# Kernel optimization log

Measured on AMD Instinct MI355X. Metric: run time of the kernel, lower is better.

The kernel has to match this reference:

```python
import jax, jax.numpy as jnp
import numpy as np


def gconv(feat, src, dst, w, n):
    # sparse weighted aggregation: out[i] = sum_{(j->i) in E} w_e * feat[j]
    return jax.ops.segment_sum(feat[src] * w[:, None], dst, num_segments=n)


def tgcn_cell(x, h, src, dst, w, Wg, bg, Wc, bc):
    n = x.shape[0]
    # gates: r, z = sigmoid(GC([x, h]) @ Wg + bg)
    a = gconv(jnp.concatenate([x, h], axis=-1), src, dst, w, n)
    rz = jax.nn.sigmoid(a @ Wg + bg)
    r, z = jnp.split(rz, 2, axis=-1)
    # candidate: c = tanh(GC([x, r*h]) @ Wc + bc)
    b = gconv(jnp.concatenate([x, r * h], axis=-1), src, dst, w, n)
    c = jnp.tanh(b @ Wc + bc)
    return z * h + (1.0 - z) * c


def setup_inputs() -> dict:
    key = jax.random.key(0)
    ks = jax.random.split(key, 8)
    N, F, T, H, E, OUT = 50000, 8, 12, 64, 800000, 1
    x = jax.random.normal(ks[0], (N, F, T), dtype=jnp.float32)
    edge_index = jax.random.randint(ks[1], (2, E), 0, N, dtype=jnp.int32)
    edge_weight = jax.random.uniform(ks[2], (E,), dtype=jnp.float32)
    init = lambda k, shp, fan: (jax.random.normal(k, shp, jnp.float32) / np.sqrt(fan)).astype(jnp.float32)
    Wg0 = init(ks[3], (F + H, 2 * H), F + H); bg0 = jnp.zeros((2 * H,), jnp.float32)
    Wc0 = init(ks[4], (F + H, H), F + H);     bc0 = jnp.zeros((H,), jnp.float32)
    Wg1 = init(ks[5], (2 * H, 2 * H), 2 * H); bg1 = jnp.zeros((2 * H,), jnp.float32)
    Wc1 = init(ks[6], (2 * H, H), 2 * H);     bc1 = jnp.zeros((H,), jnp.float32)
    Wout = init(ks[7], (H, OUT), H);          bout = jnp.zeros((OUT,), jnp.float32)
    return dict(x=x, edge_index=edge_index, edge_weight=edge_weight,
                Wg0=Wg0, bg0=bg0, Wc0=Wc0, bc0=bc0,
                Wg1=Wg1, bg1=bg1, Wc1=Wc1, bc1=bc1,
                Wout=Wout, bout=bout)


def reference(x, edge_index, edge_weight, Wg0, bg0, Wc0, bc0,
              Wg1, bg1, Wc1, bc1, Wout, bout):
    src, dst = edge_index[0], edge_index[1]
    n = x.shape[0]
    H = Wc0.shape[1]
    xt = jnp.transpose(x, (2, 0, 1))  # (T, N, F)
    h_init = (jnp.zeros((n, H), x.dtype), jnp.zeros((n, H), x.dtype))

    def step(carry, x_t):
        h0, h1 = carry
        h0 = tgcn_cell(x_t, h0, src, dst, edge_weight, Wg0, bg0, Wc0, bc0)
        h1 = tgcn_cell(h0, h1, src, dst, edge_weight, Wg1, bg1, Wc1, bc1)
        return (h0, h1), None

    (_, h1_final), _ = jax.lax.scan(step, h_init, xt)
    return h1_final @ Wout + bout  # (N, OUT); Identity output activation
```

## Files before the change

kernel.cpp:

```cpp
#include <hip/hip_runtime.h>
#include <hip/hip_fp16.h>


#define FT 96
#define TSTEPS 12

typedef _Float16 f16x8 __attribute__((ext_vector_type(8)));
typedef float f32x4 __attribute__((ext_vector_type(4)));

static __device__ __forceinline__ float lo2f(unsigned v) {
    __half2 h2 = *reinterpret_cast<const __half2*>(&v);
    return __low2float(h2);
}
static __device__ __forceinline__ float hi2f(unsigned v) {
    __half2 h2 = *reinterpret_cast<const __half2*>(&v);
    return __high2float(h2);
}
static __device__ __forceinline__ float wof(unsigned p) {
    return __half2float(__ushort_as_half((unsigned short)(p >> 16)));
}

__global__ void hist_k(const int* __restrict__ dst, int* __restrict__ deg, int E) {
    int e = blockIdx.x * blockDim.x + threadIdx.x;
    if (e < E) atomicAdd(&deg[dst[e]], 1);
}

__global__ __launch_bounds__(256) void partial_k(const int* __restrict__ deg,
                                                 int* __restrict__ part, int N) {
    __shared__ int sm[256];
    int i = blockIdx.x * 256 + threadIdx.x;
    sm[threadIdx.x] = (i < N) ? deg[i] : 0;
    __syncthreads();
    for (int off = 128; off > 0; off >>= 1) {
        if (threadIdx.x < off) sm[threadIdx.x] += sm[threadIdx.x + off];
        __syncthreads();
    }
    if (threadIdx.x == 0) part[blockIdx.x] = sm[0];
}

__global__ __launch_bounds__(256) void scanpart_k(int* __restrict__ part,
                                                  int* __restrict__ rowptr,
                                                  int G, int N) {
    __shared__ int sm[256];
    int v = (threadIdx.x < G) ? part[threadIdx.x] : 0;
    sm[threadIdx.x] = v;
    __syncthreads();
    for (int off = 1; off < 256; off <<= 1) {
        int t = (threadIdx.x >= (unsigned)off) ? sm[threadIdx.x - off] : 0;
        __syncthreads();
        sm[threadIdx.x] += t;
        __syncthreads();
    }
    if (threadIdx.x < G) part[threadIdx.x] = sm[threadIdx.x] - v;
    if (threadIdx.x == 255) rowptr[N] = sm[255];
}

__global__ __launch_bounds__(256) void scanchunk_k(const int* __restrict__ deg,
                                                   const int* __restrict__ part,
                                                   int* __restrict__ rowptr,
                                                   int* __restrict__ cursor, int N) {
    __shared__ int sm[256];
    int i = blockIdx.x * 256 + threadIdx.x;
    int v = (i < N) ? deg[i] : 0;
    sm[threadIdx.x] = v;
    __syncthreads();
    for (int off = 1; off < 256; off <<= 1) {
        int t = (threadIdx.x >= (unsigned)off) ? sm[threadIdx.x - off] : 0;
        __syncthreads();
        sm[threadIdx.x] += t;
        __syncthreads();
    }
    int excl = sm[threadIdx.x] - v + part[blockIdx.x];
    if (i < N) { rowptr[i] = excl; cursor[i] = excl; }
}

__global__ void fill_k(const int* __restrict__ src, const int* __restrict__ dst,
                       const float* __restrict__ ew, int* __restrict__ cursor,
                       unsigned* __restrict__ csr_ew, int E) {
    int e = blockIdx.x * blockDim.x + threadIdx.x;
    if (e >= E) return;
    int pos = atomicAdd(&cursor[dst[e]], 1);
    unsigned hw = (unsigned)__half_as_ushort(__float2half(ew[e]));
    csr_ew[pos] = (unsigned)src[e] | (hw << 16);
}

__global__ void x2h_k(const float* __restrict__ x, _Float16* __restrict__ xh, int M) {
    int i = blockIdx.x * blockDim.x + threadIdx.x;
    if (i < M) xh[i] = (_Float16)x[i];
}

__global__ void wprep_k(const float* __restrict__ Wg0, const float* __restrict__ Wc0,
                        const float* __restrict__ Wg1, const float* __restrict__ Wc1,
                        _Float16* __restrict__ Wg1t, _Float16* __restrict__ Wc1t,
                        _Float16* __restrict__ Wc0t, _Float16* __restrict__ Wg0t_h,
                        _Float16* __restrict__ Wg0t_x) {
    int i = blockIdx.x * 256 + threadIdx.x;
    if (i < 128 * 128) { int c = i >> 7, k = i & 127; Wg1t[i] = (_Float16)Wg1[k * 128 + c]; }
    if (i < 64 * 128)  { int c = i >> 7, k = i & 127; Wc1t[i] = (_Float16)Wc1[k * 64 + c]; }
    if (i < 64 * 96)   { int c = i / 96, k = i - c * 96;
                         Wc0t[i] = (k < 72) ? (_Float16)Wc0[k * 64 + c] : (_Float16)0.f; }
    if (i < 128 * 64)  { int c = i >> 6, k = i & 63; Wg0t_h[i] = (_Float16)Wg0[(8 + k) * 128 + c]; }
    if (i < 128 * 32)  { int c = i >> 5, k = i & 31;
                         Wg0t_x[i] = (k < 8) ? (_Float16)Wg0[k * 128 + c] : (_Float16)0.f; }
}

__global__ __launch_bounds__(256) void gather96_k(
    const _Float16* __restrict__ xh, const int* __restrict__ rowptr,
    const unsigned* __restrict__ csr_ew, float* __restrict__ aggXt, int N) {
    int n = blockIdx.x * 4 + (threadIdx.x >> 6);
    if (n >= N) return;
    int c = threadIdx.x & 63;
    int beg = rowptr[n], end = rowptr[n + 1];
    int deg = end - beg;
    float a0 = 0.f, a1 = 0.f;
    unsigned ev = 0;
    if (c < deg) ev = csr_ew[beg + c];
    int m = deg < 64 ? deg : 64;
    int m8 = (m + 7) & ~7;
#pragma unroll 8
    for (int j = 0; j < m8; ++j) {
        unsigned p = __shfl(ev, j);
        int s = p & 0xffff;
        float w = wof(p);
        const _Float16* row = xh + (size_t)s * FT;
        a0 = fmaf(w, (float)row[c], a0);
        if (c < 32) a1 = fmaf(w, (float)row[64 + c], a1);
    }
    for (int e = beg + 64; e < end; ++e) {
        unsigned p = csr_ew[e];
        int s = p & 0xffff;
        float w = wof(p);
        const _Float16* row = xh + (size_t)s * FT;
        a0 = fmaf(w, (float)row[c], a0);
        if (c < 32) a1 = fmaf(w, (float)row[64 + c], a1);
    }
    { int f = c / 12, tt = c - f * 12;
      aggXt[((size_t)tt * N + n) * 8 + f] = a0; }
    if (c < 32) { int cc = 64 + c; int f = cc / 12, tt = cc - f * 12;
      aggXt[((size_t)tt * N + n) * 8 + f] = a1; }
}

__global__ void g0z_k(const float* __restrict__ aggXt, const float* __restrict__ Wg0,
                      const float* __restrict__ bg0, _Float16* __restrict__ Zh, int N) {
    int i = blockIdx.x * blockDim.x + threadIdx.x;
    int n = i >> 6;
    if (n >= N) return;
    int c = i & 63;
    float acc = bg0[64 + c];
#pragma unroll
    for (int f = 0; f < 8; ++f) acc += aggXt[(size_t)n * 8 + f] * Wg0[f * 128 + 64 + c];
    Zh[(size_t)n * 64 + c] = (_Float16)(1.f / (1.f + __expf(-acc)));
}

__device__ __forceinline__ void gpair16(const unsigned* __restrict__ feat32,
    const unsigned* __restrict__ csr_ew,
    int begA, int degA, int begB, int degB, int lane,
    float& o0, float& o1) {
    const int half = lane >> 5, c2 = lane & 31;
    const int beg = half ? begB : begA;
    const int deg = half ? degB : degA;
    const int m = deg < 32 ? deg : 32;
    unsigned ev = 0;
    if (c2 < m) ev = csr_ew[beg + c2];
    int dmax = degA > degB ? degA : degB;
    int jm = dmax < 32 ? dmax : 32;
    jm = (jm + 15) & ~15;
    float a0 = 0.f, a1 = 0.f;
    const int base = half << 5;
    for (int j = 0; j < jm; j += 16) {
        unsigned vv[16]; float ww[16];
#pragma unroll
        for (int k = 0; k < 16; ++k) {
            unsigned p = __shfl(ev, base + j + k);
            ww[k] = wof(p);
            vv[k] = feat32[(size_t)(p & 0xffff) * 32 + c2];
        }
#pragma unroll
        for (int k = 0; k < 16; ++k) {
            a0 = fmaf(ww[k], lo2f(vv[k]), a0);
            a1 = fmaf(ww[k], hi2f(vv[k]), a1);
        }
    }
    int end = beg + deg;
    for (int e = beg + 32; e < end; ++e) {
        unsigned p = csr_ew[e];
        float w = wof(p);
        unsigned v = feat32[(size_t)(p & 0xffff) * 32 + c2];
        a0 = fmaf(w, lo2f(v), a0);
        a1 = fmaf(w, hi2f(v), a1);
    }
    o0 = a0; o1 = a1;
}

__global__ __launch_bounds__(512) void l0_cand(
    const _Float16* __restrict__ RH0h, const float* __restrict__ aggXt, int t,
    const int* __restrict__ rowptr, const unsigned* __restrict__ csr_ew,
    const _Float16* __restrict__ Wc0t, const float* __restrict__ bc,
    const _Float16* __restrict__ Zh, float* __restrict__ h0f,
    unsigned* __restrict__ h01, int N) {
    __shared__ _Float16 sA[64 * 104];
    const int tid = threadIdx.x;
    const int lane = tid & 63;
    const int wid = __builtin_amdgcn_readfirstlane(tid >> 6);
    const int nb = blockIdx.x * 64;
    { int nl = tid >> 3, k0 = 72 + ((tid & 7) << 2);
#pragma unroll
      for (int q = 0; q < 4; ++q) sA[nl * 104 + k0 + q] = (_Float16)0.f; }
    { int nl = tid >> 3, f = tid & 7, n = nb + nl;
      sA[nl * 104 + f] = (n < N) ? (_Float16)aggXt[((size_t)t * N + n) * 8 + f] : (_Float16)0.f; }
    for (int i = 0; i < 4; ++i) {
        int pr = wid * 4 + i;
        int nlA = pr * 2, nlB = nlA + 1;
        int nA = nb + nlA, nB = nb + nlB;
        int begA = 0, degA = 0, begB = 0, degB = 0;
        if (nA < N) { begA = rowptr[nA]; degA = rowptr[nA + 1] - begA; }
        if (nB < N) { begB = rowptr[nB]; degB = rowptr[nB + 1] - begB; }
        float o0, o1;
        gpair16((const unsigned*)RH0h, csr_ew, begA, degA, begB, degB, lane, o0, o1);
        int nl = (lane < 32) ? nlA : nlB;
        int c2 = lane & 31;
        sA[nl * 104 + 8 + 2 * c2] = (_Float16)o0;
        sA[nl * 104 + 8 + 2 * c2 + 1] = (_Float16)o1;
    }
    __syncthreads();
    const int ln15 = lane & 15, quad = lane >> 4;
    const int mt = wid & 3, ng = wid >> 2;
    const int mrow = mt * 16 + ln15;
    f16x8 afr[3];
#pragma unroll
    for (int kc = 0; kc < 3; ++kc)
        afr[kc] = *(const f16x8*)&sA[mrow * 104 + kc * 32 + quad * 8];
    f32x4 acc[2];
    int cols[2];
#pragma unroll
    for (int nt = 0; nt < 2; ++nt) {
        int col = (ng * 2 + nt) * 16 + ln15;
        cols[nt] = col;
        float b = bc[col];
        f32x4 a = {b, b, b, b};
#pragma unroll
        for (int kc = 0; kc < 3; ++kc) {
            f16x8 bfr = *(const f16x8*)&Wc0t[(size_t)col * 96 + kc * 32 + quad * 8];
            a = __builtin_amdgcn_mfma_f32_16x16x32_f16(afr[kc], bfr, a, 0, 0, 0);
        }
        acc[nt] = a;
    }
    __syncthreads();
#pragma unroll
    for (int nt = 0; nt < 2; ++nt) {
#pragma unroll
        for (int r = 0; r < 4; ++r) {
            float e = __expf(2.f * acc[nt][r]);
            float c = 1.f - 2.f / (e + 1.f);
            int row = mt * 16 + quad * 4 + r;
            sA[row * 104 + cols[nt]] = (_Float16)c;
        }
    }
    __syncthreads();
    for (int i = tid; i < 4096; i += 512) {
        int nl = i >> 6, cc = i & 63, n = nb + nl;
        if (n < N) {
            size_t idx = (size_t)n * 64 + cc;
            float z = (float)Zh[idx];
            float hv = h0f[idx];
            float nh = z * hv + (1.f - z) * (float)sA[nl * 104 + cc];
            h0f[idx] = nh;
            reinterpret_cast<__half*>(h01)[idx * 2] = __float2half(nh);
        }
    }
}

__global__ __launch_bounds__(512) void l1_gate(
    const unsigned* __restrict__ h01, const float* __restrict__ h1f,
    const int* __restrict__ rowptr, const unsigned* __restrict__ csr_ew,
    const _Float16* __restrict__ Wg1t, const float* __restrict__ bg,
    unsigned* __restrict__ Aglobh32, _Float16* __restrict__ Zh,
    _Float16* __restrict__ RH1h, int N) {
    __shared__ _Float16 sA[64 * 136];
    const int tid = threadIdx.x;
    const int lane = tid & 63;
    const int wid = __builtin_amdgcn_readfirstlane(tid >> 6);
    const int nb = blockIdx.x * 64;
    const uint2* __restrict__ f2 = (const uint2*)h01;
    for (int i = 0; i < 4; ++i) {
        int pr = wid * 4 + i;
        int nlA = pr * 2, nlB = nlA + 1;
        int nA = nb + nlA, nB = nb + nlB;
        int begA = 0, degA = 0, begB = 0, degB = 0;
        if (nA < N) { begA = rowptr[nA]; degA = rowptr[nA + 1] - begA; }
        if (nB < N) { begB = rowptr[nB]; degB = rowptr[nB + 1] - begB; }
        const int half = lane >> 5, c2 = lane & 31;
        const int beg = half ? begB : begA;
        const int deg = half ? degB : degA;
        const int m = deg < 32 ? deg : 32;
        unsigned ev = 0;
        if (c2 < m) ev = csr_ew[beg + c2];
        int dmax = degA > degB ? degA : degB;
        int jm = dmax < 32 ? dmax : 32;
        jm = (jm + 7) & ~7;
        float p00 = 0.f, p01 = 0.f, p10 = 0.f, p11 = 0.f;
        const int base = half << 5;
        for (int j = 0; j < jm; j += 8) {
            uint2 vv[8]; float ww[8];
#pragma unroll
            for (int k = 0; k < 8; ++k) {
                unsigned p = __shfl(ev, base + j + k);
                ww[k] = wof(p);
                vv[k] = f2[(size_t)(p & 0xffff) * 32 + c2];
            }
#pragma unroll
            for (int k = 0; k < 8; ++k) {
                p00 = fmaf(ww[k], lo2f(vv[k].x), p00);
                p10 = fmaf(ww[k], hi2f(vv[k].x), p10);
                p01 = fmaf(ww[k], lo2f(vv[k].y), p01);
                p11 = fmaf(ww[k], hi2f(vv[k].y), p11);
            }
        }
        int end = beg + deg;
        for (int e = beg + 32; e < end; ++e) {
            unsigned p = csr_ew[e];
            float w = wof(p);
            uint2 v = f2[(size_t)(p & 0xffff) * 32 + c2];
            p00 = fmaf(w, lo2f(v.x), p00);
            p10 = fmaf(w, hi2f(v.x), p10);
            p01 = fmaf(w, lo2f(v.y), p01);
            p11 = fmaf(w, hi2f(v.y), p11);
        }
        int nl = (lane < 32) ? nlA : nlB;
        int c2w = lane & 31;
        sA[nl * 136 + 2 * c2w] = (_Float16)p00;
        sA[nl * 136 + 2 * c2w + 1] = (_Float16)p01;
        sA[nl * 136 + 64 + 2 * c2w] = (_Float16)p10;
        sA[nl * 136 + 64 + 2 * c2w + 1] = (_Float16)p11;
    }
    __syncthreads();
    for (int i = tid; i < 2048; i += 512) {
        int nl = i >> 5, c2 = i & 31, n = nb + nl;
        if (n < N) Aglobh32[(size_t)n * 32 + c2] = ((const unsigned*)sA)[nl * 68 + c2];
    }
    const int ln15 = lane & 15, quad = lane >> 4;
    const int mt = wid & 3, ng = wid >> 2;
    const int mrow = mt * 16 + ln15;
    f16x8 afr[4];
#pragma unroll
    for (int kc = 0; kc < 4; ++kc)
        afr[kc] = *(const f16x8*)&sA[mrow * 136 + kc * 32 + quad * 8];
    f32x4 acc[4];
    int cols[4];
#pragma unroll
    for (int nt = 0; nt < 4; ++nt) {
        int col = (ng * 4 + nt) * 16 + ln15;
        cols[nt] = col;
        float b = bg[col];
        f32x4 a = {b, b, b, b};
#pragma unroll
        for (int kc = 0; kc < 4; ++kc) {
            f16x8 bfr = *(const f16x8*)&Wg1t[(size_t)col * 128 + kc * 32 + quad * 8];
            a = __builtin_amdgcn_mfma_f32_16x16x32_f16(afr[kc], bfr, a, 0, 0, 0);
        }
        acc[nt] = a;
    }
    __syncthreads();
#pragma unroll
    for (int nt = 0; nt < 4; ++nt) {
#pragma unroll
        for (int r = 0; r < 4; ++r) {
            float s = 1.f / (1.f + __expf(-acc[nt][r]));
            int row = mt * 16 + quad * 4 + r;
            sA[row * 136 + cols[nt]] = (_Float16)s;
        }
    }
    __syncthreads();
    for (int i = tid; i < 4096; i += 512) {
        int nl = i >> 6, cc = i & 63, n = nb + nl;
        if (n < N) {
            size_t idx = (size_t)n * 64 + cc;
            float r = (float)sA[nl * 136 + cc];
            float z = (float)sA[nl * 136 + 64 + cc];
            RH1h[idx] = (_Float16)(r * h1f[idx]);
            Zh[idx] = (_Float16)z;
        }
    }
}

__global__ __launch_bounds__(512) void l1_cand_fused(
    const _Float16* __restrict__ RH1h, const unsigned* __restrict__ Aglobh32,
    const float* __restrict__ aggXt, int tn, int do_gate, int final,
    const int* __restrict__ rowptr, const unsigned* __restrict__ csr_ew,
    const _Float16* __restrict__ Wc1t, const float* __restrict__ bc1,
    const _Float16* __restrict__ Wg0t_h, const _Float16* __restrict__ Wg0t_x,
    const float* __restrict__ bg0, const float* __restrict__ h0f,
    _Float16* __restrict__ Zh, _Float16* __restrict__ RH0h,
    float* __restrict__ h1f, unsigned* __restrict__ h01,
    const float* __restrict__ Wout, const float* __restrict__ bout,
    float* __restrict__ out, int N) {
    __shared__ _Float16 sA[64 * 136];
    __shared__ _Float16 sX[64 * 40];
    const int tid = threadIdx.x;
    const int lane = tid & 63;
    const int wid = __builtin_amdgcn_readfirstlane(tid >> 6);
    const int nb = blockIdx.x * 64;
    { int nl = tid >> 3, k0 = 8 + ((tid & 7) << 2);
#pragma unroll
      for (int q = 0; q < 4; ++q) sX[nl * 40 + k0 + q] = (_Float16)0.f; }
    if (do_gate) {
        int nl = tid >> 3, f = tid & 7, n = nb + nl;
        sX[nl * 40 + f] = (n < N) ? (_Float16)aggXt[((size_t)tn * N + n) * 8 + f] : (_Float16)0.f;
    }
    for (int i = tid; i < 2048; i += 512) {
        int nl = i >> 5, c2 = i & 31, n = nb + nl;
        ((unsigned*)sA)[nl * 68 + c2] = (n < N) ? Aglobh32[(size_t)n * 32 + c2] : 0u;
    }
    for (int i = 0; i < 4; ++i) {
        int pr = wid * 4 + i;
        int nlA = pr * 2, nlB = nlA + 1;
        int nA = nb + nlA, nB = nb + nlB;
        int begA = 0, degA = 0, begB = 0, degB = 0;
        if (nA < N) { begA = rowptr[nA]; degA = rowptr[nA + 1] - begA; }
        if (nB < N) { begB = rowptr[nB]; degB = rowptr[nB + 1] - begB; }
        float o0, o1;
        gpair16((const unsigned*)RH1h, csr_ew, begA, degA, begB, degB, lane, o0, o1);
        int nl = (lane < 32) ? nlA : nlB;
        int c2 = lane & 31;
        sA[nl * 136 + 64 + 2 * c2] = (_Float16)o0;
        sA[nl * 136 + 64 + 2 * c2 + 1] = (_Float16)o1;
    }
    __syncthreads();
    const int ln15 = lane & 15, quad = lane >> 4;
    const int mt = wid & 3, ng = wid >> 2;
    const int mrow = mt * 16 + ln15;
    f16x8 afr[4];
#pragma unroll
    for (int kc = 0; kc < 4; ++kc)
        afr[kc] = *(const f16x8*)&sA[mrow * 136 + kc * 32 + quad * 8];
    f32x4 accc[2];
    int colc[2];
#pragma unroll
    for (int nt = 0; nt < 2; ++nt) {
        int col = (ng * 2 + nt) * 16 + ln15;
        colc[nt] = col;
        float b = bc1[col];
        f32x4 a = {b, b, b, b};
#pragma unroll
        for (int kc = 0; kc < 4; ++kc) {
            f16x8 bfr = *(const f16x8*)&Wc1t[(size_t)col * 128 + kc * 32 + quad * 8];
            a = __builtin_amdgcn_mfma_f32_16x16x32_f16(afr[kc], bfr, a, 0, 0, 0);
        }
        accc[nt] = a;
    }
    f32x4 accg[4];
    int colg[4];
    if (do_gate) {
        f16x8 xfr = *(const f16x8*)&sX[mrow * 40 + quad * 8];
#pragma unroll
        for (int nt = 0; nt < 4; ++nt) {
            int col = (ng * 4 + nt) * 16 + ln15;
            colg[nt] = col;
            float b = bg0[col];
            f32x4 a = {b, b, b, b};
            f16x8 bx = *(const f16x8*)&Wg0t_x[(size_t)col * 32 + quad * 8];
            a = __builtin_amdgcn_mfma_f32_16x16x32_f16(xfr, bx, a, 0, 0, 0);
#pragma unroll
            for (int kc = 0; kc < 2; ++kc) {
                f16x8 bfr = *(const f16x8*)&Wg0t_h[(size_t)col * 64 + kc * 32 + quad * 8];
                a = __builtin_amdgcn_mfma_f32_16x16x32_f16(afr[kc], bfr, a, 0, 0, 0);
            }
            accg[nt] = a;
        }
    }
    __syncthreads();
#pragma unroll
    for (int nt = 0; nt < 2; ++nt) {
#pragma unroll
        for (int r = 0; r < 4; ++r) {
            float e = __expf(2.f * accc[nt][r]);
            float c = 1.f - 2.f / (e + 1.f);
            int row = mt * 16 + quad * 4 + r;
            sA[row * 136 + 64 + colc[nt]] = (_Float16)c;
        }
    }
    if (do_gate) {
#pragma unroll
        for (int nt = 0; nt < 4; ++nt) {
            if (colg[nt] < 64) {
#pragma unroll
                for (int r = 0; r < 4; ++r) {
                    float s = 1.f / (1.f + __expf(-accg[nt][r]));
                    int row = mt * 16 + quad * 4 + r;
                    sA[row * 136 + colg[nt]] = (_Float16)s;
                }
            }
        }
    }
    __syncthreads();
    for (int i = tid; i < 4096; i += 512) {
        int nl = i >> 6, cc = i & 63, n = nb + nl;
        float nh = 0.f;
        if (n < N) {
            size_t idx = (size_t)n * 64 + cc;
            float z1 = (float)Zh[idx];
            float hv = h1f[idx];
            nh = z1 * hv + (1.f - z1) * (float)sA[nl * 136 + 64 + cc];
            if (!final) {
                h1f[idx] = nh;
                reinterpret_cast<__half*>(h01)[idx * 2 + 1] = __float2half(nh);
            }
            if (do_gate) RH0h[idx] = (_Float16)((float)sA[nl * 136 + cc] * h0f[idx]);
        }
        if (final) {
            float p = nh * Wout[cc];
            for (int off = 32; off > 0; off >>= 1) p += __shfl_down(p, off);
            if (cc == 0 && n < N) out[n] = p + bout[0];
        }
    }
    if (do_gate) {
        __syncthreads();
#pragma unroll
        for (int nt = 0; nt < 4; ++nt) {
            if (colg[nt] >= 64) {
#pragma unroll
                for (int r = 0; r < 4; ++r) {
                    float s = 1.f / (1.f + __expf(-accg[nt][r]));
                    int row = mt * 16 + quad * 4 + r;
                    sA[row * 136 + (colg[nt] - 64)] = (_Float16)s;
                }
            }
        }
        __syncthreads();
        for (int i = tid; i < 4096; i += 512) {
            int nl = i >> 6, cc = i & 63, n = nb + nl;
            if (n < N) Zh[(size_t)n * 64 + cc] = sA[nl * 136 + cc];
        }
    }
}

static inline size_t align16(size_t v) { return (v + 15) & ~(size_t)15; }

extern "C" void kernel_launch(void* const* d_in, const int* in_sizes, int n_in,
                              void* d_out, int out_size, void* d_ws, size_t ws_size,
                              hipStream_t stream) {
    const float* x   = (const float*)d_in[0];
    const int*   ei  = (const int*)d_in[1];
    const float* ew  = (const float*)d_in[2];
    const float* Wg0 = (const float*)d_in[3];
    const float* bg0 = (const float*)d_in[4];
    const float* Wc0 = (const float*)d_in[5];
    const float* bc0 = (const float*)d_in[6];
    const float* Wg1 = (const float*)d_in[7];
    const float* bg1 = (const float*)d_in[8];
    const float* Wc1 = (const float*)d_in[9];
    const float* bc1 = (const float*)d_in[10];
    const float* Wout = (const float*)d_in[11];
    const float* bout = (const float*)d_in[12];

    const int N = in_sizes[0] / FT;
    const int E = in_sizes[2];
    const int* src = ei;
    const int* dst = ei + E;

    char* base = (char*)d_ws;
    size_t off = 0;
    int* deg = (int*)(base + off);            off = align16(off + (size_t)N * 4);
    int* cursor = (int*)(base + off);         off = align16(off + (size_t)N * 4);
    int* rowptr = (int*)(base + off);         off = align16(off + (size_t)(N + 1) * 4);
    int* part = (int*)(base + off);           off = align16(off + 256 * 4);
    unsigned* csr_ew = (unsigned*)(base + off);  off = align16(off + (size_t)E * 4);
    float* aggXt = (float*)(base + off);      off = align16(off + (size_t)N * FT * 4);
    float* h0f = (float*)(base + off);        off = align16(off + (size_t)N * 64 * 4);
    float* h1f = (float*)(base + off);        off = align16(off + (size_t)N * 64 * 4);
    unsigned* h01 = (unsigned*)(base + off);  off = align16(off + (size_t)N * 64 * 4);
    unsigned* Aglobh32 = (unsigned*)(base + off); off = align16(off + (size_t)N * 32 * 4);
    _Float16* Zh = (_Float16*)(base + off);   off = align16(off + (size_t)N * 64 * 2);
    _Float16* RH0h = (_Float16*)(base + off); off = align16(off + (size_t)N * 64 * 2);
    _Float16* RH1h = (_Float16*)(base + off); off = align16(off + (size_t)N * 64 * 2);
    _Float16* xh = (_Float16*)(base + off);   off = align16(off + (size_t)N * FT * 2);
    _Float16* Wg1t = (_Float16*)(base + off); off = align16(off + 128 * 128 * 2);
    _Float16* Wc1t = (_Float16*)(base + off); off = align16(off + 64 * 128 * 2);
    _Float16* Wc0t = (_Float16*)(base + off); off = align16(off + 64 * 96 * 2);
    _Float16* Wg0t_h = (_Float16*)(base + off); off = align16(off + 128 * 64 * 2);
    _Float16* Wg0t_x = (_Float16*)(base + off); off = align16(off + 128 * 32 * 2);

    const int gE   = (E + 255) / 256;
    const int gN4  = (N + 3) / 4;
    const int gN64 = (N + 63) / 64;
    const int G    = (N + 255) / 256;

    hipMemsetAsync(deg, 0, (size_t)N * 4, stream);
    hipMemsetAsync(h0f, 0, (size_t)N * 64 * 4, stream);
    hipMemsetAsync(h1f, 0, (size_t)N * 64 * 4, stream);
    hipMemsetAsync(h01, 0, (size_t)N * 64 * 4, stream);
    hipMemsetAsync(RH0h, 0, (size_t)N * 64 * 2, stream);

    x2h_k<<<(N * FT + 255) / 256, 256, 0, stream>>>(x, xh, N * FT);
    wprep_k<<<64, 256, 0, stream>>>(Wg0, Wc0, Wg1, Wc1, Wg1t, Wc1t, Wc0t, Wg0t_h, Wg0t_x);
    hist_k<<<gE, 256, 0, stream>>>(dst, deg, E);
    partial_k<<<G, 256, 0, stream>>>(deg, part, N);
    scanpart_k<<<1, 256, 0, stream>>>(part, rowptr, G, N);
    scanchunk_k<<<G, 256, 0, stream>>>(deg, part, rowptr, cursor, N);
    fill_k<<<gE, 256, 0, stream>>>(src, dst, ew, cursor, csr_ew, E);
    gather96_k<<<gN4, 256, 0, stream>>>(xh, rowptr, csr_ew, aggXt, N);

    g0z_k<<<(N * 64 + 255) / 256, 256, 0, stream>>>(aggXt, Wg0, bg0, Zh, N);

    for (int t = 0; t < TSTEPS; ++t) {
        l0_cand<<<gN64, 512, 0, stream>>>(RH0h, aggXt, t, rowptr, csr_ew,
                                          Wc0t, bc0, Zh, h0f, h01, N);
        l1_gate<<<gN64, 512, 0, stream>>>(h01, h1f, rowptr, csr_ew,
                                          Wg1t, bg1, Aglobh32, Zh, RH1h, N);
        l1_cand_fused<<<gN64, 512, 0, stream>>>(RH1h, Aglobh32, aggXt, t + 1,
                                                (t + 1 < TSTEPS) ? 1 : 0,
                                                (t + 1 == TSTEPS) ? 1 : 0,
                                                rowptr, csr_ew,
                                                Wc1t, bc1, Wg0t_h, Wg0t_x, bg0,
                                                h0f, Zh, RH0h, h1f, h01,
                                                Wout, bout, (float*)d_out, N);
    }
}
```

Before: 1.965 ms.

## Sort nodes by degree and gather four nodes per wavefront with wider loads

Adds a degree-bucketed node permutation (histogram, scan, fill) so each 64-node block and each wavefront processes nodes of similar in-degree, cutting divergence and padded iterations in the neighbour gather loops. The gather is also reorganized from two nodes per wave with 32 lanes each to four nodes per wave with 16 lanes each, loading wider vectors (uint2/uint4) per lane and packing results into half2 LDS stores. All row-indexed global reads and writes now go through perm, which makes them scattered, and three small setup kernels are added.

```diff
diff --git a/kernel.cpp b/kernel.cpp
--- a/kernel.cpp
+++ b/kernel.cpp
@@ -18,6 +18,10 @@
 }
 static __device__ __forceinline__ float wof(unsigned p) {
     return __half2float(__ushort_as_half((unsigned short)(p >> 16)));
+}
+static __device__ __forceinline__ unsigned packh2(float a, float b) {
+    __half2 h = __floats2half2_rn(a, b);
+    return *reinterpret_cast<unsigned*>(&h);
 }
 
 __global__ void hist_k(const int* __restrict__ dst, int* __restrict__ deg, int E) {
@@ -82,6 +86,26 @@
     int pos = atomicAdd(&cursor[dst[e]], 1);
     unsigned hw = (unsigned)__half_as_ushort(__float2half(ew[e]));
     csr_ew[pos] = (unsigned)src[e] | (hw << 16);
+}
+
+__global__ void deghist_k(const int* __restrict__ deg, int* __restrict__ bins, int N) {
+    int n = blockIdx.x * blockDim.x + threadIdx.x;
+    if (n < N) { int d = deg[n]; atomicAdd(&bins[d > 63 ? 63 : d], 1); }
+}
+__global__ void binscan_k(int* __restrict__ bins) {
+    if (threadIdx.x == 0) {
+        int acc = 0;
+        for (int i = 0; i < 64; ++i) { int v = bins[i]; bins[i] = acc; acc += v; }
+    }
+}
+__global__ void permfill_k(const int* __restrict__ deg, int* __restrict__ bins,
+                           int* __restrict__ perm, int N) {
+    int n = blockIdx.x * blockDim.x + threadIdx.x;
+    if (n < N) {
+        int d = deg[n];
+        int pos = atomicAdd(&bins[d > 63 ? 63 : d], 1);
+        perm[pos] = n;
+    }
 }
 
 __global__ void x2h_k(const float* __restrict__ x, _Float16* __restrict__ xh, int M) {
@@ -152,49 +176,52 @@
     Zh[(size_t)n * 64 + c] = (_Float16)(1.f / (1.f + __expf(-acc)));
 }
 
-__device__ __forceinline__ void gpair16(const unsigned* __restrict__ feat32,
-    const unsigned* __restrict__ csr_ew,
-    int begA, int degA, int begB, int degB, int lane,
-    float& o0, float& o1) {
-    const int half = lane >> 5, c2 = lane & 31;
-    const int beg = half ? begB : begA;
-    const int deg = half ? degB : degA;
-    const int m = deg < 32 ? deg : 32;
-    unsigned ev = 0;
-    if (c2 < m) ev = csr_ew[beg + c2];
-    int dmax = degA > degB ? degA : degB;
-    int jm = dmax < 32 ? dmax : 32;
+__device__ __forceinline__ void gquad1(const uint2* __restrict__ f2,
+    const unsigned* __restrict__ csr_ew, int beg, int deg, int c4, int lb,
+    float& a0, float& a1, float& a2, float& a3) {
+    int m = deg < 32 ? deg : 32;
+    unsigned ev0 = 0, ev1 = 0;
+    if (c4 < m) ev0 = csr_ew[beg + c4];
+    if (16 + c4 < m) ev1 = csr_ew[beg + 16 + c4];
+    int dm = deg;
+    dm = max(dm, __shfl_xor(dm, 16));
+    dm = max(dm, __shfl_xor(dm, 32));
+    int jm = dm < 32 ? dm : 32;
     jm = (jm + 15) & ~15;
-    float a0 = 0.f, a1 = 0.f;
-    const int base = half << 5;
-    for (int j = 0; j < jm; j += 16) {
-        unsigned vv[16]; float ww[16];
+    a0 = a1 = a2 = a3 = 0.f;
+    for (int j0 = 0; j0 < jm; j0 += 16) {
+        unsigned e = j0 ? ev1 : ev0;
+        uint2 vv[16]; float ww[16];
 #pragma unroll
         for (int k = 0; k < 16; ++k) {
-            unsigned p = __shfl(ev, base + j + k);
+            unsigned p = __shfl(e, lb + k);
             ww[k] = wof(p);
-            vv[k] = feat32[(size_t)(p & 0xffff) * 32 + c2];
+            vv[k] = f2[(size_t)(p & 0xffff) * 16 + c4];
         }
 #pragma unroll
         for (int k = 0; k < 16; ++k) {
-            a0 = fmaf(ww[k], lo2f(vv[k]), a0);
-            a1 = fmaf(ww[k], hi2f(vv[k]), a1);
+            a0 = fmaf(ww[k], lo2f(vv[k].x), a0);
+            a1 = fmaf(ww[k], hi2f(vv[k].x), a1);
+            a2 = fmaf(ww[k], lo2f(vv[k].y), a2);
+            a3 = fmaf(ww[k], hi2f(vv[k].y), a3);
         }
     }
     int end = beg + deg;
     for (int e = beg + 32; e < end; ++e) {
         unsigned p = csr_ew[e];
         float w = wof(p);
-        unsigned v = feat32[(size_t)(p & 0xffff) * 32 + c2];
-        a0 = fmaf(w, lo2f(v), a0);
-        a1 = fmaf(w, hi2f(v), a1);
-    }
-    o0 = a0; o1 = a1;
+        uint2 v = f2[(size_t)(p & 0xffff) * 16 + c4];
+        a0 = fmaf(w, lo2f(v.x), a0);
+        a1 = fmaf(w, hi2f(v.x), a1);
+        a2 = fmaf(w, lo2f(v.y), a2);
+        a3 = fmaf(w, hi2f(v.y), a3);
+    }
 }
 
 __global__ __launch_bounds__(512) void l0_cand(
     const _Float16* __restrict__ RH0h, const float* __restrict__ aggXt, int t,
     const int* __restrict__ rowptr, const unsigned* __restrict__ csr_ew,
+    const int* __restrict__ perm,
     const _Float16* __restrict__ Wc0t, const float* __restrict__ bc,
     const _Float16* __restrict__ Zh, float* __restrict__ h0f,
     unsigned* __restrict__ h01, int N) {
@@ -206,21 +233,20 @@
     { int nl = tid >> 3, k0 = 72 + ((tid & 7) << 2);
 #pragma unroll
       for (int q = 0; q < 4; ++q) sA[nl * 104 + k0 + q] = (_Float16)0.f; }
-    { int nl = tid >> 3, f = tid & 7, n = nb + nl;
-      sA[nl * 104 + f] = (n < N) ? (_Float16)aggXt[((size_t)t * N + n) * 8 + f] : (_Float16)0.f; }
-    for (int i = 0; i < 4; ++i) {
-        int pr = wid * 4 + i;
-        int nlA = pr * 2, nlB = nlA + 1;
-        int nA = nb + nlA, nB = nb + nlB;
-        int begA = 0, degA = 0, begB = 0, degB = 0;
-        if (nA < N) { begA = rowptr[nA]; degA = rowptr[nA + 1] - begA; }
-        if (nB < N) { begB = rowptr[nB]; degB = rowptr[nB + 1] - begB; }
-        float o0, o1;
-        gpair16((const unsigned*)RH0h, csr_ew, begA, degA, begB, degB, lane, o0, o1);
-        int nl = (lane < 32) ? nlA : nlB;
-        int c2 = lane & 31;
-        sA[nl * 104 + 8 + 2 * c2] = (_Float16)o0;
-        sA[nl * 104 + 8 + 2 * c2 + 1] = (_Float16)o1;
+    { int nl = tid >> 3, f = tid & 7, gi = nb + nl;
+      int n = (gi < N) ? perm[gi] : -1;
+      sA[nl * 104 + f] = (n >= 0) ? (_Float16)aggXt[((size_t)t * N + n) * 8 + f] : (_Float16)0.f; }
+    const int c4 = lane & 15, lb = lane & 48, q = lane >> 4;
+    const uint2* f2 = (const uint2*)RH0h;
+    for (int it = 0; it < 2; ++it) {
+        int nl = (wid * 2 + it) * 4 + q;
+        int gi = nb + nl;
+        int beg = 0, deg = 0;
+        if (gi < N) { int n = perm[gi]; beg = rowptr[n]; deg = rowptr[n + 1] - beg; }
+        float a0, a1, a2, a3;
+        gquad1(f2, csr_ew, beg, deg, c4, lb, a0, a1, a2, a3);
+        uint2 u; u.x = packh2(a0, a1); u.y = packh2(a2, a3);
+        *(uint2*)&sA[nl * 104 + 8 + 4 * c4] = u;
     }
     __syncthreads();
     const int ln15 = lane & 15, quad = lane >> 4;
@@ -258,8 +284,9 @@
     }
     __syncthreads();
     for (int i = tid; i < 4096; i += 512) {
-        int nl = i >> 6, cc = i & 63, n = nb + nl;
-        if (n < N) {
+        int nl = i >> 6, cc = i & 63, gi = nb + nl;
+        if (gi < N) {
+            int n = perm[gi];
             size_t idx = (size_t)n * 64 + cc;
             float z = (float)Zh[idx];
             float hv = h0f[idx];
@@ -273,6 +300,7 @@
 __global__ __launch_bounds__(512) void l1_gate(
     const unsigned* __restrict__ h01, const float* __restrict__ h1f,
     const int* __restrict__ rowptr, const unsigned* __restrict__ csr_ew,
+    const int* __restrict__ perm,
     const _Float16* __restrict__ Wg1t, const float* __restrict__ bg,
     unsigned* __restrict__ Aglobh32, _Float16* __restrict__ Zh,
     _Float16* __restrict__ RH1h, int N) {
@@ -281,62 +309,61 @@
     const int lane = tid & 63;
     const int wid = __builtin_amdgcn_readfirstlane(tid >> 6);
     const int nb = blockIdx.x * 64;
-    const uint2* __restrict__ f2 = (const uint2*)h01;
-    for (int i = 0; i < 4; ++i) {
-        int pr = wid * 4 + i;
-        int nlA = pr * 2, nlB = nlA + 1;
-        int nA = nb + nlA, nB = nb + nlB;
-        int begA = 0, degA = 0, begB = 0, degB = 0;
-        if (nA < N) { begA = rowptr[nA]; degA = rowptr[nA + 1] - begA; }
-        if (nB < N) { begB = rowptr[nB]; degB = rowptr[nB + 1] - begB; }
-        const int half = lane >> 5, c2 = lane & 31;
-        const int beg = half ? begB : begA;
-        const int deg = half ? degB : degA;
-        const int m = deg < 32 ? deg : 32;
-        unsigned ev = 0;
-        if (c2 < m) ev = csr_ew[beg + c2];
-        int dmax = degA > degB ? degA : degB;
-        int jm = dmax < 32 ? dmax : 32;
+    const int c4 = lane & 15, lb = lane & 48, q = lane >> 4;
+    const uint4* __restrict__ f4 = (const uint4*)h01;
+    for (int it = 0; it < 2; ++it) {
+        int nl = (wid * 2 + it) * 4 + q;
+        int gi = nb + nl;
+        int beg = 0, deg = 0;
+        if (gi < N) { int n = perm[gi]; beg = rowptr[n]; deg = rowptr[n + 1] - beg; }
+        int m = deg < 32 ? deg : 32;
+        unsigned ev0 = 0, ev1 = 0;
+        if (c4 < m) ev0 = csr_ew[beg + c4];
+        if (16 + c4 < m) ev1 = csr_ew[beg + 16 + c4];
+        int dm = deg;
+        dm = max(dm, __shfl_xor(dm, 16));
+        dm = max(dm, __shfl_xor(dm, 32));
+        int jm = dm < 32 ? dm : 32;
         jm = (jm + 7) & ~7;
-        float p00 = 0.f, p01 = 0.f, p10 = 0.f, p11 = 0.f;
-        const int base = half << 5;
-        for (int j = 0; j < jm; j += 8) {
-            uint2 vv[8]; float ww[8];
+        float b0 = 0.f, b1 = 0.f, b2 = 0.f, b3 = 0.f;
+        float c0 = 0.f, c1 = 0.f, c2 = 0.f, c3 = 0.f;
+        for (int j0 = 0; j0 < jm; j0 += 8) {
+            unsigned e = (j0 < 16) ? ev0 : ev1;
+            int bs = j0 & 15;
+            uint4 vv[8]; float ww[8];
 #pragma unroll
             for (int k = 0; k < 8; ++k) {
-                unsigned p = __shfl(ev, base + j + k);
+                unsigned p = __shfl(e, lb + bs + k);
                 ww[k] = wof(p);
-                vv[k] = f2[(size_t)(p & 0xffff) * 32 + c2];
+                vv[k] = f4[(size_t)(p & 0xffff) * 16 + c4];
             }
 #pragma unroll
             for (int k = 0; k < 8; ++k) {
-                p00 = fmaf(ww[k], lo2f(vv[k].x), p00);
-                p10 = fmaf(ww[k], hi2f(vv[k].x), p10);
-                p01 = fmaf(ww[k], lo2f(vv[k].y), p01);
-                p11 = fmaf(ww[k], hi2f(vv[k].y), p11);
+                b0 = fmaf(ww[k], lo2f(vv[k].x), b0); c0 = fmaf(ww[k], hi2f(vv[k].x), c0);
+                b1 = fmaf(ww[k], lo2f(vv[k].y), b1); c1 = fmaf(ww[k], hi2f(vv[k].y), c1);
+                b2 = fmaf(ww[k], lo2f(vv[k].z), b2); c2 = fmaf(ww[k], hi2f(vv[k].z), c2);
+                b3 = fmaf(ww[k], lo2f(vv[k].w), b3); c3 = fmaf(ww[k], hi2f(vv[k].w), c3);
             }
         }
         int end = beg + deg;
         for (int e = beg + 32; e < end; ++e) {
             unsigned p = csr_ew[e];
             float w = wof(p);
-            uint2 v = f2[(size_t)(p & 0xffff) * 32 + c2];
-            p00 = fmaf(w, lo2f(v.x), p00);
-            p10 = fmaf(w, hi2f(v.x), p10);
-            p01 = fmaf(w, lo2f(v.y), p01);
-            p11 = fmaf(w, hi2f(v.y), p11);
-        }
-        int nl = (lane < 32) ? nlA : nlB;
-        int c2w = lane & 31;
-        sA[nl * 136 + 2 * c2w] = (_Float16)p00;
-        sA[nl * 136 + 2 * c2w + 1] = (_Float16)p01;
-        sA[nl * 136 + 64 + 2 * c2w] = (_Float16)p10;
-        sA[nl * 136 + 64 + 2 * c2w + 1] = (_Float16)p11;
+            uint4 v = f4[(size_t)(p & 0xffff) * 16 + c4];
+            b0 = fmaf(w, lo2f(v.x), b0); c0 = fmaf(w, hi2f(v.x), c0);
+            b1 = fmaf(w, lo2f(v.y), b1); c1 = fmaf(w, hi2f(v.y), c1);
+            b2 = fmaf(w, lo2f(v.z), b2); c2 = fmaf(w, hi2f(v.z), c2);
+            b3 = fmaf(w, lo2f(v.w), b3); c3 = fmaf(w, hi2f(v.w), c3);
+        }
+        uint2 u0; u0.x = packh2(b0, b1); u0.y = packh2(b2, b3);
+        uint2 u1; u1.x = packh2(c0, c1); u1.y = packh2(c2, c3);
+        *(uint2*)&sA[nl * 136 + 4 * c4] = u0;
+        *(uint2*)&sA[nl * 136 + 64 + 4 * c4] = u1;
     }
     __syncthreads();
     for (int i = tid; i < 2048; i += 512) {
-        int nl = i >> 5, c2 = i & 31, n = nb + nl;
-        if (n < N) Aglobh32[(size_t)n * 32 + c2] = ((const unsigned*)sA)[nl * 68 + c2];
+        int nl = i >> 5, c2 = i & 31, gi = nb + nl;
+        if (gi < N) Aglobh32[(size_t)perm[gi] * 32 + c2] = ((const unsigned*)sA)[nl * 68 + c2];
     }
     const int ln15 = lane & 15, quad = lane >> 4;
     const int mt = wid & 3, ng = wid >> 2;
@@ -372,9 +399,9 @@
     }
     __syncthreads();
     for (int i = tid; i < 4096; i += 512) {
-        int nl = i >> 6, cc = i & 63, n = nb + nl;
-        if (n < N) {
-            size_t idx = (size_t)n * 64 + cc;
+        int nl = i >> 6, cc = i & 63, gi = nb + nl;
+        if (gi < N) {
+            size_t idx = (size_t)perm[gi] * 64 + cc;
             float r = (float)sA[nl * 136 + cc];
             float z = (float)sA[nl * 136 + 64 + cc];
             RH1h[idx] = (_Float16)(r * h1f[idx]);
@@ -387,6 +414,7 @@
     const _Float16* __restrict__ RH1h, const unsigned* __restrict__ Aglobh32,
     const float* __restrict__ aggXt, int tn, int do_gate, int final,
     const int* __restrict__ rowptr, const unsigned* __restrict__ csr_ew,
+    const int* __restrict__ perm,
     const _Float16* __restrict__ Wc1t, const float* __restrict__ bc1,
     const _Float16* __restrict__ Wg0t_h, const _Float16* __restrict__ Wg0t_x,
     const float* __restrict__ bg0, const float* __restrict__ h0f,
@@ -404,26 +432,25 @@
 #pragma unroll
       for (int q = 0; q < 4; ++q) sX[nl * 40 + k0 + q] = (_Float16)0.f; }
     if (do_gate) {
-        int nl = tid >> 3, f = tid & 7, n = nb + nl;
-        sX[nl * 40 + f] = (n < N) ? (_Float16)aggXt[((size_t)tn * N + n) * 8 + f] : (_Float16)0.f;
+        int nl = tid >> 3, f = tid & 7, gi = nb + nl;
+        int n = (gi < N) ? perm[gi] : -1;
+        sX[nl * 40 + f] = (n >= 0) ? (_Float16)aggXt[((size_t)tn * N + n) * 8 + f] : (_Float16)0.f;
     }
     for (int i = tid; i < 2048; i += 512) {
-        int nl = i >> 5, c2 = i & 31, n = nb + nl;
-        ((unsigned*)sA)[nl * 68 + c2] = (n < N) ? Aglobh32[(size_t)n * 32 + c2] : 0u;
-    }
-    for (int i = 0; i < 4; ++i) {
-        int pr = wid * 4 + i;
-        int nlA = pr * 2, nlB = nlA + 1;
-        int nA = nb + nlA, nB = nb + nlB;
-        int begA = 0, degA = 0, begB = 0, degB = 0;
-        if (nA < N) { begA = rowptr[nA]; degA = rowptr[nA + 1] - begA; }
-        if (nB < N) { begB = rowptr[nB]; degB = rowptr[nB + 1] - begB; }
-        float o0, o1;
-        gpair16((const unsigned*)RH1h, csr_ew, begA, degA, begB, degB, lane, o0, o1);
-        int nl = (lane < 32) ? nlA : nlB;
-        int c2 = lane & 31;
-        sA[nl * 136 + 64 + 2 * c2] = (_Float16)o0;
-        sA[nl * 136 + 64 + 2 * c2 + 1] = (_Float16)o1;
+        int nl = i >> 5, c2 = i & 31, gi = nb + nl;
+        ((unsigned*)sA)[nl * 68 + c2] = (gi < N) ? Aglobh32[(size_t)perm[gi] * 32 + c2] : 0u;
+    }
+    const int c4 = lane & 15, lb = lane & 48, q = lane >> 4;
+    const uint2* f2 = (const uint2*)RH1h;
+    for (int it = 0; it < 2; ++it) {
+        int nl = (wid * 2 + it) * 4 + q;
+        int gi = nb + nl;
+        int beg = 0, deg = 0;
+        if (gi < N) { int n = perm[gi]; beg = rowptr[n]; deg = rowptr[n + 1] - beg; }
+        float a0, a1, a2, a3;
+        gquad1(f2, csr_ew, beg, deg, c4, lb, a0, a1, a2, a3);
+        uint2 u; u.x = packh2(a0, a1); u.y = packh2(a2, a3);
+        *(uint2*)&sA[nl * 136 + 64 + 4 * c4] = u;
     }
     __syncthreads();
     const int ln15 = lane & 15, quad = lane >> 4;
@@ -494,9 +521,11 @@
     }
     __syncthreads();
     for (int i = tid; i < 4096; i += 512) {
-        int nl = i >> 6, cc = i & 63, n = nb + nl;
+        int nl = i >> 6, cc = i & 63, gi = nb + nl;
         float nh = 0.f;
-        if (n < N) {
+        int n = -1;
+        if (gi < N) {
+            n = perm[gi];
             size_t idx = (size_t)n * 64 + cc;
             float z1 = (float)Zh[idx];
             float hv = h1f[idx];
@@ -510,7 +539,7 @@
         if (final) {
             float p = nh * Wout[cc];
             for (int off = 32; off > 0; off >>= 1) p += __shfl_down(p, off);
-            if (cc == 0 && n < N) out[n] = p + bout[0];
+            if (cc == 0 && n >= 0) out[n] = p + bout[0];
         }
     }
     if (do_gate) {
@@ -528,8 +557,8 @@
         }
         __syncthreads();
         for (int i = tid; i < 4096; i += 512) {
-            int nl = i >> 6, cc = i & 63, n = nb + nl;
-            if (n < N) Zh[(size_t)n * 64 + cc] = sA[nl * 136 + cc];
+            int nl = i >> 6, cc = i & 63, gi = nb + nl;
+            if (gi < N) Zh[(size_t)perm[gi] * 64 + cc] = sA[nl * 136 + cc];
         }
     }
 }
@@ -564,6 +593,8 @@
     int* cursor = (int*)(base + off);         off = align16(off + (size_t)N * 4);
     int* rowptr = (int*)(base + off);         off = align16(off + (size_t)(N + 1) * 4);
     int* part = (int*)(base + off);           off = align16(off + 256 * 4);
+    int* bins = (int*)(base + off);           off = align16(off + 64 * 4);
+    int* perm = (int*)(base + off);           off = align16(off + (size_t)N * 4);
     unsigned* csr_ew = (unsigned*)(base + off);  off = align16(off + (size_t)E * 4);
     float* aggXt = (float*)(base + off);      off = align16(off + (size_t)N * FT * 4);
     float* h0f = (float*)(base + off);        off = align16(off + (size_t)N * 64 * 4);
@@ -584,8 +615,10 @@
     const int gN4  = (N + 3) / 4;
     const int gN64 = (N + 63) / 64;
     const int G    = (N + 255) / 256;
+    const int gNn  = (N + 255) / 256;
 
     hipMemsetAsync(deg, 0, (size_t)N * 4, stream);
+    hipMemsetAsync(bins, 0, 64 * 4, stream);
     hipMemsetAsync(h0f, 0, (size_t)N * 64 * 4, stream);
     hipMemsetAsync(h1f, 0, (size_t)N * 64 * 4, stream);
     hipMemsetAsync(h01, 0, (size_t)N * 64 * 4, stream);
@@ -598,19 +631,22 @@
     scanpart_k<<<1, 256, 0, stream>>>(part, rowptr, G, N);
     scanchunk_k<<<G, 256, 0, stream>>>(deg, part, rowptr, cursor, N);
     fill_k<<<gE, 256, 0, stream>>>(src, dst, ew, cursor, csr_ew, E);
+    deghist_k<<<gNn, 256, 0, stream>>>(deg, bins, N);
+    binscan_k<<<1, 64, 0, stream>>>(bins);
+    permfill_k<<<gNn, 256, 0, stream>>>(deg, bins, perm, N);
     gather96_k<<<gN4, 256, 0, stream>>>(xh, rowptr, csr_ew, aggXt, N);
 
     g0z_k<<<(N * 64 + 255) / 256, 256, 0, stream>>>(aggXt, Wg0, bg0, Zh, N);
 
     for (int t = 0; t < TSTEPS; ++t) {
-        l0_cand<<<gN64, 512, 0, stream>>>(RH0h, aggXt, t, rowptr, csr_ew,
+        l0_cand<<<gN64, 512, 0, stream>>>(RH0h, aggXt, t, rowptr, csr_ew, perm,
                                           Wc0t, bc0, Zh, h0f, h01, N);
-        l1_gate<<<gN64, 512, 0, stream>>>(h01, h1f, rowptr, csr_ew,
+        l1_gate<<<gN64, 512, 0, stream>>>(h01, h1f, rowptr, csr_ew, perm,
                                           Wg1t, bg1, Aglobh32, Zh, RH1h, N);
         l1_cand_fused<<<gN64, 512, 0, stream>>>(RH1h, Aglobh32, aggXt, t + 1,
                                                 (t + 1 < TSTEPS) ? 1 : 0,
                                                 (t + 1 == TSTEPS) ? 1 : 0,
-                                                rowptr, csr_ew,
+                                                rowptr, csr_ew, perm,
                                                 Wc1t, bc1, Wg0t_h, Wg0t_x, bg0,
                                                 h0f, Zh, RH0h, h1f, h01,
                                                 Wout, bout, (float*)d_out, N);
```

Result: slower. 2.710 ms (+37.9%).
